# Performance work log

Hardware: AMD Instinct MI355X
Metric: run time of the kernel (lower is better)

Reference implementation:

```python
import jax, jax.numpy as jnp
import numpy as np

B, N, D, H = 4, 2048, 256, 4
NT, ET = 5, 6
HEAD = D // H


def _linear_params(k, fan_in, fan_out):
    # torch nn.Linear default init: U(-1/sqrt(fan_in), 1/sqrt(fan_in)) for W and b
    bound = 1.0 / np.sqrt(fan_in)
    kw, kb = jax.random.split(k)
    W = jax.random.uniform(kw, (fan_in, fan_out), minval=-bound, maxval=bound, dtype=jnp.float32)
    b = jax.random.uniform(kb, (fan_out,), minval=-bound, maxval=bound, dtype=jnp.float32)
    return W, b


def setup_inputs() -> dict:
    key = jax.random.key(0)
    ks = jax.random.split(key, 10)
    Wq, bq = _linear_params(ks[0], D, D)
    Wk, bk = _linear_params(ks[1], D, D)
    Wv, bv = _linear_params(ks[2], D, D)
    Wo, bo = _linear_params(ks[3], D, D)
    return {
        "nodes": jax.random.normal(ks[4], (B, N, D), dtype=jnp.float32),
        "node_types": jax.random.randint(ks[5], (B, N), 0, NT, dtype=jnp.int32),
        "edge_types": jax.random.randint(ks[6], (B, N, N), 0, ET, dtype=jnp.int32),
        "adjacency": jax.random.randint(ks[7], (B, N, N), 0, 2).astype(jnp.float32),
        "node_type_embed": jax.random.normal(ks[8], (NT, D), dtype=jnp.float32),  # nn.Embedding ~ N(0,1)
        "edge_type_embed": jax.random.normal(ks[9], (ET, H), dtype=jnp.float32),
        "Wq": Wq, "bq": bq, "Wk": Wk, "bk": bk, "Wv": Wv, "bv": bv, "Wo": Wo, "bo": bo,
        "ln_g": jnp.ones((D,), jnp.float32),
        "ln_b": jnp.zeros((D,), jnp.float32),
    }


def reference(nodes, node_types, edge_types, adjacency, node_type_embed, edge_type_embed,
              Wq, bq, Wk, bk, Wv, bv, Wo, bo, ln_g, ln_b):
    # add node-type embeddings (residual below uses the typed nodes, as in the torch code)
    x = nodes + node_type_embed[node_types]                      # [B,N,D]

    def split_heads(t):
        return t.reshape(B, N, H, HEAD).transpose(0, 2, 1, 3)    # [B,H,N,HEAD]

    Q = split_heads(x @ Wq + bq)
    K = split_heads(x @ Wk + bk)
    V = split_heads(x @ Wv + bv)

    scores = jnp.einsum('bhnd,bhmd->bhnm', Q, K) / np.sqrt(HEAD).astype(np.float32)

    # edge-type bias: [B,N,N,H] -> [B,H,N,N]
    scores = scores + jnp.transpose(edge_type_embed[edge_types], (0, 3, 1, 2))

    # type-match soft mask: match -> +0.1, mismatch -> -0.05  (== tm*0.15 - 0.05)
    tm = (node_types[:, :, None] == node_types[:, None, :]).astype(jnp.float32)
    scores = scores + (tm * 0.15 - 0.05)[:, None]

    # adjacency hard mask
    scores = scores + ((1.0 - adjacency) * -1e9)[:, None]

    attn = jax.nn.softmax(scores, axis=-1)                        # [B,H,N,N]
    ctx = jnp.einsum('bhnm,bhmd->bhnd', attn, V)
    ctx = ctx.transpose(0, 2, 1, 3).reshape(B, N, D)

    out = ctx @ Wo + bo
    y = x + out
    mu = jnp.mean(y, axis=-1, keepdims=True)
    var = jnp.var(y, axis=-1, keepdims=True)
    y = (y - mu) * jax.lax.rsqrt(var + 1e-5) * ln_g + ln_b
    return y, attn
```

## Files before the change

### kernel.cpp

```cpp
#include <hip/hip_runtime.h>

#define Bsz 4
#define Nn 2048
#define Dd 256
#define Hh 4
#define HD 64
#define NTt 5
#define ETt 6
#define LOG2E 1.4426950408889634f
#define MSUB 24.0f
#define SCLQ 0.18033688011112042f

typedef float f32x4 __attribute__((ext_vector_type(4)));
typedef __bf16 bf16x8 __attribute__((ext_vector_type(8)));
typedef unsigned int u32x4 __attribute__((ext_vector_type(4)));
typedef short s16x4 __attribute__((ext_vector_type(4)));
typedef unsigned short u16;
typedef unsigned char u8;
typedef unsigned int uint;

static __device__ __forceinline__ u16 f2bf(float f) {
  unsigned int u = __builtin_bit_cast(unsigned int, f);
  u = (u + 0x7fffu + ((u >> 16) & 1u)) >> 16;
  return (u16)u;
}

static __device__ __forceinline__ bf16x8 ld8(const u16* p) {
  return __builtin_bit_cast(bf16x8, *(const u32x4*)p);
}

static __device__ __forceinline__ void stage16(const void* g, void* l) {
  __builtin_amdgcn_global_load_lds(
      (const __attribute__((address_space(1))) uint*)g,
      (__attribute__((address_space(3))) uint*)l, 16, 0, 0);
}

#define MFMA16(a, b, c) __builtin_amdgcn_mfma_f32_16x16x32_bf16((a), (b), (c), 0, 0, 0)

#define OFF_X      0u
#define OFF_XBF    8388608u
#define OFF_WQKVT  12582912u
#define OFF_WOT    12976128u
#define OFF_BQKV   13107200u
#define OFF_Q      13110272u
#define OFF_K      17304576u
#define OFF_V      21498880u
#define OFF_VT     25693184u
#define OFF_CTX    29887488u
#define OFF_CODES  34081792u

__global__ void pack_kernel(const float* Wq, const float* Wk, const float* Wv,
                            const float* Wo, const float* bq, const float* bk,
                            const float* bv, u16* wqkvT, u16* woT, float* bqkv) {
  int tid = blockIdx.x * 256 + threadIdx.x;
  if (tid < 196608) {
    int c = tid >> 8, k = tid & 255;
    int which = c >> 8, cc = c & 255;
    const float* W = (which == 0) ? Wq : ((which == 1) ? Wk : Wv);
    wqkvT[tid] = f2bf(W[k * 256 + cc]);
  } else if (tid < 262144) {
    int t2 = tid - 196608;
    int c = t2 >> 8, k = t2 & 255;
    woT[t2] = f2bf(Wo[k * 256 + c]);
  } else if (tid < 262912) {
    int c = tid - 262144;
    int which = c >> 8, cc = c & 255;
    bqkv[c] = (which == 0) ? bq[cc] : ((which == 1) ? bk[cc] : bv[cc]);
  }
}

__global__ void embed_kernel(const float* nodes, const int* node_types,
                             const float* nte, float* xf, u16* xbf) {
  int t = blockIdx.x * 256 + threadIdx.x;
  int flat = t * 4;
  int bn = flat >> 8, d0 = flat & 255;
  int nt = node_types[bn];
  float4 nv = *(const float4*)(nodes + flat);
  float4 ev = *(const float4*)(nte + nt * 256 + d0);
  float4 x4;
  x4.x = nv.x + ev.x; x4.y = nv.y + ev.y; x4.z = nv.z + ev.z; x4.w = nv.w + ev.w;
  *(float4*)(xf + flat) = x4;
  ushort4 xb;
  xb.x = f2bf(x4.x); xb.y = f2bf(x4.y); xb.z = f2bf(x4.z); xb.w = f2bf(x4.w);
  *(ushort4*)(xbf + flat) = xb;
}

__global__ __launch_bounds__(256) void maskpack_kernel(
    const int* node_types, const int* edge_types, const float* adjacency,
    u8* codes) {
  int t = blockIdx.x * 256 + threadIdx.x;
  int lane = t & 63;
  int kt = (t >> 6) & 31;
  int qt = (t >> 11) & 127;
  int b = t >> 18;
  int l15 = lane & 15, l4 = lane >> 4;
  const int* etb = edge_types + (size_t)b * Nn * Nn;
  const float* adjb = adjacency + (size_t)b * Nn * Nn;
  const int* ntb = node_types + b * Nn;
  int qrow = qt * 16 + l15;
  int ntq = ntb[qrow];
  const int* etr = etb + (size_t)qrow * Nn;
  const float* adr = adjb + (size_t)qrow * Nn;
  unsigned int wds[4];
#pragma unroll
  for (int ks = 0; ks < 4; ++ks) {
    int k0 = kt * 64 + ks * 16 + l4 * 4;
    int4 et4 = *(const int4*)(etr + k0);
    float4 a4 = *(const float4*)(adr + k0);
    int4 nt4 = *(const int4*)(ntb + k0);
    int e[4] = {et4.x, et4.y, et4.z, et4.w};
    int n[4] = {nt4.x, nt4.y, nt4.z, nt4.w};
    float a[4] = {a4.x, a4.y, a4.z, a4.w};
    unsigned int acc = 0;
#pragma unroll
    for (int j = 0; j < 4; ++j) {
      int code = e[j] + ((ntq == n[j]) ? 6 : 0) + ((a[j] != 0.0f) ? 12 : 0);
      acc |= (unsigned int)(code * 4) << (8 * j);
    }
    wds[ks] = acc;
  }
  u32x4 out = {wds[0], wds[1], wds[2], wds[3]};
  *(u32x4*)(codes + (size_t)t * 16) = out;
}

__global__ __launch_bounds__(256) void qkv_kernel(const u16* xbf, const u16* wqkvT,
                                                  const float* bqkv,
                                                  u16* Qb, u16* Kb, u16* Vb) {
  int cb = blockIdx.x;
  int rb = blockIdx.y;
  int w = threadIdx.x >> 6, lane = threadIdx.x & 63;
  int l15 = lane & 15, l4 = lane >> 4;
  int row0 = rb * 64 + w * 16;
  int col0 = cb * 64;
  const u16* xr = xbf + (size_t)(row0 + l15) * 256;
  f32x4 acc[4];
#pragma unroll
  for (int i = 0; i < 4; ++i) acc[i] = (f32x4){0.f, 0.f, 0.f, 0.f};
#pragma unroll
  for (int kst = 0; kst < 8; ++kst) {
    int k0 = kst * 32 + l4 * 8;
    bf16x8 a = ld8(xr + k0);
#pragma unroll
    for (int cs = 0; cs < 4; ++cs) {
      int col = col0 + cs * 16 + l15;
      bf16x8 bw = ld8(wqkvT + (size_t)col * 256 + k0);
      acc[cs] = MFMA16(a, bw, acc[cs]);
    }
  }
#pragma unroll
  for (int cs = 0; cs < 4; ++cs) {
    int col = col0 + cs * 16 + l15;
    float bias = bqkv[col];
    int which = col >> 8, c = col & 255;
    int h = c >> 6, hd = c & 63;
    float scale = (which == 0) ? SCLQ : 1.0f;
    u16* dst = (which == 0) ? Qb : ((which == 1) ? Kb : Vb);
#pragma unroll
    for (int j = 0; j < 4; ++j) {
      int row = row0 + l4 * 4 + j;
      int bb = row >> 11, n = row & 2047;
      dst[(size_t)(((bb * Hh + h) * Nn + n)) * HD + hd] = f2bf((acc[cs][j] + bias) * scale);
    }
  }
}

__global__ __launch_bounds__(256) void vtrans_kernel(const u16* Vb, u16* Vtb) {
  int bh = blockIdx.y;
  int d = threadIdx.x & 63;
  int nc = threadIdx.x >> 6;
  int n0 = blockIdx.x * 64 + nc * 16;
  const u16* Vp = Vb + (size_t)bh * Nn * HD;
  union { u16 a[16]; u32x4 v[2]; } tmp;
#pragma unroll
  for (int i = 0; i < 16; ++i) tmp.a[i] = Vp[(size_t)(n0 + i) * HD + d];
  u16* dst = Vtb + ((size_t)bh * HD + d) * Nn + n0;
  *(u32x4*)dst = tmp.v[0];
  *(u32x4*)(dst + 8) = tmp.v[1];
}

__global__ __launch_bounds__(256) void attn_kernel(
    const u16* Qb, const u16* Kb, const u16* Vtb, const u8* codes,
    const float* ee_g, float* attn_out, u16* ctx_ws) {
  __shared__ __align__(16) char kls[2][8192];
  __shared__ __align__(16) char vls[2][8192];
  __shared__ __align__(16) char pls[4][2048];

  int bid0 = blockIdx.x;
  int bid = ((bid0 & 7) << 6) | (bid0 >> 3);
  int qt64 = bid & 31;
  int h = (bid >> 5) & 3;
  int b = bid >> 7;
  int w = threadIdx.x >> 6, lane = threadIdx.x & 63;
  int l15 = lane & 15, l4 = lane >> 4;
  int q0 = qt64 * 64 + w * 16;

  float lutv = 0.f;
  {
    int ln = lane;
    int et = ln - 6 * (ln / 6);
    int tm = (ln / 6) & 1;
    int adj = ln / 12;
    if (ln < 24)
      lutv = (ee_g[et * Hh + h] + (tm ? 0.10f : -0.05f)) * LOG2E +
             (adj ? 0.f : -1.442695041e9f) - MSUB;
  }
  int lut_i = __float_as_int(lutv);

  const u16* Qp = Qb + (size_t)((b * Hh + h) * Nn + q0 + l15) * HD;
  bf16x8 bq0 = ld8(Qp + l4 * 8);
  bf16x8 bq1 = ld8(Qp + 32 + l4 * 8);

  const char* Kg = (const char*)(Kb + (size_t)(b * Hh + h) * Nn * HD);
  const char* Vg = (const char*)(Vtb + (size_t)(b * Hh + h) * HD * Nn);
  const u32x4* cp = (const u32x4*)codes + ((size_t)(b * 128 + (q0 >> 4)) * 32) * 64;

  int oT0 = w * 2048 + lane * 16;
  int oT1 = oT0 + 1024;
  int ksw0 = oT0 ^ (((oT0 >> 7) & 7) << 4);
  int ksw1 = oT1 ^ (((oT1 >> 7) & 7) << 4);
  const char* VgR0 = Vg + (size_t)(oT0 >> 7) * (Nn * 2) + (ksw0 & 127);
  const char* VgR1 = Vg + (size_t)(oT1 >> 7) * (Nn * 2) + (ksw1 & 127);

  int sw = (l15 & 7) << 4;
  int ra = (l15 * 128 + l4 * 16) ^ sw;
  int qa = q0 + l15;

  stage16(Kg + ksw0, (char*)kls + w * 2048);
  stage16(Kg + ksw1, (char*)kls + w * 2048 + 1024);
  u32x4 cw = cp[lane];
  __syncthreads();

  float accl = 0.f;
#pragma unroll 1
  for (int kt = 0; kt < 32; ++kt) {
    int cb = kt & 1, nb = cb ^ 1;
    u32x4 cwn = cw;
    if (kt < 31) {
      const char* Kn = Kg + (size_t)(kt + 1) * 8192;
      stage16(Kn + ksw0, (char*)kls + nb * 8192 + w * 2048);
      stage16(Kn + ksw1, (char*)kls + nb * 8192 + w * 2048 + 1024);
      cwn = cp[(kt + 1) * 64 + lane];
    }
    __builtin_amdgcn_sched_barrier(0);
    const char* kcur = (const char*)kls + cb * 8192;
#pragma unroll
    for (int ks = 0; ks < 4; ++ks) {
      unsigned int cword = cw[ks];
      f32x4 acc;
#pragma unroll
      for (int j = 0; j < 4; ++j) {
        int c4 = (cword >> (8 * j)) & 0xFF;
        acc[j] = __int_as_float(__builtin_amdgcn_ds_bpermute(c4, lut_i));
      }
      acc = MFMA16(ld8((const u16*)(kcur + ra + ks * 2048)), bq0, acc);
      acc = MFMA16(ld8((const u16*)(kcur + (ra ^ 64) + ks * 2048)), bq1, acc);
      accl += (__builtin_amdgcn_exp2f(acc[0]) + __builtin_amdgcn_exp2f(acc[1])) +
              (__builtin_amdgcn_exp2f(acc[2]) + __builtin_amdgcn_exp2f(acc[3]));
    }
    asm volatile("s_waitcnt vmcnt(1) lgkmcnt(0)" ::: "memory");
    __builtin_amdgcn_s_barrier();
    cw = cwn;
  }
  accl += __shfl_xor(accl, 16);
  accl += __shfl_xor(accl, 32);
  bool zrow = (accl == 0.0f);
  float pscale = zrow ? 0.0f : 1.0f / accl;
  float pbias = zrow ? (1.0f / 2048.0f) : 0.0f;

  float* attb = attn_out + (size_t)(b * Hh + h) * Nn * Nn + (size_t)qa * Nn;
  char* pwave = (char*)pls + w * 2048;
  int pwbase = l15 * 128;
  f32x4 ctx[4];
#pragma unroll
  for (int i = 0; i < 4; ++i) ctx[i] = (f32x4){0.f, 0.f, 0.f, 0.f};

  stage16(Kg + ksw0, (char*)kls + w * 2048);
  stage16(Kg + ksw1, (char*)kls + w * 2048 + 1024);
  stage16(VgR0, (char*)vls + w * 2048);
  stage16(VgR1, (char*)vls + w * 2048 + 1024);
  cw = cp[lane];
  __syncthreads();

#pragma unroll 1
  for (int kt = 0; kt < 32; ++kt) {
    int cb = kt & 1, nb = cb ^ 1;
    u32x4 cwn = cw;
    if (kt < 31) {
      const char* Kn = Kg + (size_t)(kt + 1) * 8192;
      stage16(Kn + ksw0, (char*)kls + nb * 8192 + w * 2048);
      stage16(Kn + ksw1, (char*)kls + nb * 8192 + w * 2048 + 1024);
      stage16(VgR0 + (size_t)(kt + 1) * 128, (char*)vls + nb * 8192 + w * 2048);
      stage16(VgR1 + (size_t)(kt + 1) * 128, (char*)vls + nb * 8192 + w * 2048 + 1024);
      cwn = cp[(kt + 1) * 64 + lane];
    }
    __builtin_amdgcn_sched_barrier(0);
    const char* kcur = (const char*)kls + cb * 8192;
    const char* vcur = (const char*)vls + cb * 8192;
#pragma unroll
    for (int ks = 0; ks < 4; ++ks) {
      unsigned int cword = cw[ks];
      f32x4 acc;
#pragma unroll
      for (int j = 0; j < 4; ++j) {
        int c4 = (cword >> (8 * j)) & 0xFF;
        acc[j] = __int_as_float(__builtin_amdgcn_ds_bpermute(c4, lut_i));
      }
      acc = MFMA16(ld8((const u16*)(kcur + ra + ks * 2048)), bq0, acc);
      acc = MFMA16(ld8((const u16*)(kcur + (ra ^ 64) + ks * 2048)), bq1, acc);
      f32x4 p;
#pragma unroll
      for (int j = 0; j < 4; ++j)
        p[j] = __builtin_amdgcn_exp2f(acc[j]) * pscale + pbias;
      __builtin_nontemporal_store(p, (f32x4*)(attb + kt * 64 + ks * 16 + l4 * 4));
      s16x4 pb;
#pragma unroll
      for (int j = 0; j < 4; ++j)
        pb[j] = (short)__builtin_bit_cast(u16, (__bf16)p[j]);
      *(s16x4*)(pwave + pwbase + ((ks * 32 + l4 * 8) ^ sw)) = pb;
    }
    bf16x8 pa0 = ld8((const u16*)(pwave + pwbase + ((l4 * 16) ^ sw)));
    bf16x8 pa1 = ld8((const u16*)(pwave + pwbase + ((l4 * 16 + 64) ^ sw)));
#pragma unroll
    for (int ds_ = 0; ds_ < 4; ++ds_) {
      bf16x8 v0 = ld8((const u16*)(vcur + ra + ds_ * 2048));
      bf16x8 v1 = ld8((const u16*)(vcur + (ra ^ 64) + ds_ * 2048));
      ctx[ds_] = MFMA16(pa0, v0, ctx[ds_]);
      ctx[ds_] = MFMA16(pa1, v1, ctx[ds_]);
    }
    asm volatile("s_waitcnt vmcnt(5) lgkmcnt(0)" ::: "memory");
    __builtin_amdgcn_s_barrier();
    cw = cwn;
  }

#pragma unroll
  for (int ds_ = 0; ds_ < 4; ++ds_) {
    int col = h * 64 + ds_ * 16 + l15;
#pragma unroll
    for (int j = 0; j < 4; ++j) {
      int qrow = q0 + l4 * 4 + j;
      ctx_ws[(size_t)(b * Nn + qrow) * Dd + col] = f2bf(ctx[ds_][j]);
    }
  }
}

__global__ __launch_bounds__(256) void outln_kernel(const u16* ctxb, const u16* woT,
                                                    const float* bo, const float* xf,
                                                    const float* ln_g, const float* ln_b,
                                                    float* yout) {
  __shared__ float ytile[32][257];
  __shared__ float muS[32], rvS[32];
  int bm0 = blockIdx.x * 32;
  int w = threadIdx.x >> 6, lane = threadIdx.x & 63;
  int l15 = lane & 15, l4 = lane >> 4;
  f32x4 acc[2][4];
#pragma unroll
  for (int q = 0; q < 2; ++q)
#pragma unroll
    for (int i = 0; i < 4; ++i) acc[q][i] = (f32x4){0.f, 0.f, 0.f, 0.f};
#pragma unroll
  for (int kst = 0; kst < 8; ++kst) {
    int k0 = kst * 32 + l4 * 8;
    bf16x8 a0 = ld8(ctxb + (size_t)(bm0 + l15) * 256 + k0);
    bf16x8 a1 = ld8(ctxb + (size_t)(bm0 + 16 + l15) * 256 + k0);
#pragma unroll
    for (int ds_ = 0; ds_ < 4; ++ds_) {
      bf16x8 bw = ld8(woT + (size_t)(w * 64 + ds_ * 16 + l15) * 256 + k0);
      acc[0][ds_] = MFMA16(a0, bw, acc[0][ds_]);
      acc[1][ds_] = MFMA16(a1, bw, acc[1][ds_]);
    }
  }
#pragma unroll
  for (int qs = 0; qs < 2; ++qs)
#pragma unroll
    for (int ds_ = 0; ds_ < 4; ++ds_) {
      int col = w * 64 + ds_ * 16 + l15;
      float bof = bo[col];
#pragma unroll
      for (int j = 0; j < 4; ++j) {
        int row = qs * 16 + l4 * 4 + j;
        ytile[row][col] = acc[qs][ds_][j] + bof + xf[(size_t)(bm0 + row) * 256 + col];
      }
    }
  __syncthreads();
  int row = threadIdx.x >> 3, seg = threadIdx.x & 7;
  float ps = 0.f, pq = 0.f;
#pragma unroll
  for (int c = 0; c < 32; ++c) {
    float v = ytile[row][seg * 32 + c];
    ps += v; pq += v * v;
  }
  ps += __shfl_xor(ps, 1); pq += __shfl_xor(pq, 1);
  ps += __shfl_xor(ps, 2); pq += __shfl_xor(pq, 2);
  ps += __shfl_xor(ps, 4); pq += __shfl_xor(pq, 4);
  if (seg == 0) {
    float mu = ps * (1.0f / 256.0f);
    muS[row] = mu;
    rvS[row] = rsqrtf(pq * (1.0f / 256.0f) - mu * mu + 1e-5f);
  }
  __syncthreads();
  float mu = muS[row], rv = rvS[row];
  float* yr = yout + (size_t)(bm0 + row) * 256;
#pragma unroll
  for (int c0 = 0; c0 < 32; c0 += 4) {
    int c = seg * 32 + c0;
    float4 o;
    o.x = (ytile[row][c + 0] - mu) * rv * ln_g[c + 0] + ln_b[c + 0];
    o.y = (ytile[row][c + 1] - mu) * rv * ln_g[c + 1] + ln_b[c + 1];
    o.z = (ytile[row][c + 2] - mu) * rv * ln_g[c + 2] + ln_b[c + 2];
    o.w = (ytile[row][c + 3] - mu) * rv * ln_g[c + 3] + ln_b[c + 3];
    *(float4*)(yr + c) = o;
  }
}

extern "C" void kernel_launch(void* const* d_in, const int* in_sizes, int n_in,
                              void* d_out, int out_size, void* d_ws, size_t ws_size,
                              hipStream_t stream) {
  const float* nodes = (const float*)d_in[0];
  const int* node_types = (const int*)d_in[1];
  const int* edge_types = (const int*)d_in[2];
  const float* adjacency = (const float*)d_in[3];
  const float* nte = (const float*)d_in[4];
  const float* ee = (const float*)d_in[5];
  const float* Wq = (const float*)d_in[6];
  const float* bq = (const float*)d_in[7];
  const float* Wk = (const float*)d_in[8];
  const float* bk = (const float*)d_in[9];
  const float* Wv = (const float*)d_in[10];
  const float* bv = (const float*)d_in[11];
  const float* Wo = (const float*)d_in[12];
  const float* bo = (const float*)d_in[13];
  const float* ln_g = (const float*)d_in[14];
  const float* ln_b = (const float*)d_in[15];

  float* y = (float*)d_out;
  float* attn = y + (size_t)Bsz * Nn * Dd;

  char* ws = (char*)d_ws;
  float* xf = (float*)(ws + OFF_X);
  u16* xbf = (u16*)(ws + OFF_XBF);
  u16* wqkvT = (u16*)(ws + OFF_WQKVT);
  u16* woT = (u16*)(ws + OFF_WOT);
  float* bqkv = (float*)(ws + OFF_BQKV);
  u16* Qb = (u16*)(ws + OFF_Q);
  u16* Kb = (u16*)(ws + OFF_K);
  u16* Vb = (u16*)(ws + OFF_V);
  u16* Vtb = (u16*)(ws + OFF_VT);
  u16* ctxb = (u16*)(ws + OFF_CTX);
  u8* codes = (u8*)(ws + OFF_CODES);

  pack_kernel<<<1027, 256, 0, stream>>>(Wq, Wk, Wv, Wo, bq, bk, bv, wqkvT, woT, bqkv);
  embed_kernel<<<2048, 256, 0, stream>>>(nodes, node_types, nte, xf, xbf);
  maskpack_kernel<<<4096, 256, 0, stream>>>(node_types, edge_types, adjacency, codes);
  qkv_kernel<<<dim3(12, 128), 256, 0, stream>>>(xbf, wqkvT, bqkv, Qb, Kb, Vb);
  vtrans_kernel<<<dim3(32, 16), 256, 0, stream>>>(Vb, Vtb);
  attn_kernel<<<512, 256, 0, stream>>>(Qb, Kb, Vtb, codes, ee, attn, ctxb);
  outln_kernel<<<256, 256, 0, stream>>>(ctxb, woT, bo, xf, ln_g, ln_b, y);
}
```

Measured before the change: 193.2 us.

## Use single-wave attention blocks loading K/V directly from global; fuse V transpose into QKV

The attention kernel becomes one 64-thread wave per 16-query tile, loading K and V fragments straight from global memory into registers instead of double-buffering them through LDS with barriers. The V transpose kernel is removed: the QKV projection now writes V directly in transposed layout. This drops one launch and all block-level syncs and LDS staging. In exchange, K/V reuse across the four waves of a block is lost, so more global/L2 traffic is generated, and the transposed V stores are scattered.

```diff
diff --git a/kernel.cpp b/kernel.cpp
--- a/kernel.cpp
+++ b/kernel.cpp
@@ -27,12 +27,6 @@
 
 static __device__ __forceinline__ bf16x8 ld8(const u16* p) {
   return __builtin_bit_cast(bf16x8, *(const u32x4*)p);
-}
-
-static __device__ __forceinline__ void stage16(const void* g, void* l) {
-  __builtin_amdgcn_global_load_lds(
-      (const __attribute__((address_space(1))) uint*)g,
-      (__attribute__((address_space(3))) uint*)l, 16, 0, 0);
 }
 
 #define MFMA16(a, b, c) __builtin_amdgcn_mfma_f32_16x16x32_bf16((a), (b), (c), 0, 0, 0)
@@ -125,7 +119,7 @@
 
 __global__ __launch_bounds__(256) void qkv_kernel(const u16* xbf, const u16* wqkvT,
                                                   const float* bqkv,
-                                                  u16* Qb, u16* Kb, u16* Vb) {
+                                                  u16* Qb, u16* Kb, u16* Vtb) {
   int cb = blockIdx.x;
   int rb = blockIdx.y;
   int w = threadIdx.x >> 6, lane = threadIdx.x & 63;
@@ -154,45 +148,35 @@
     int which = col >> 8, c = col & 255;
     int h = c >> 6, hd = c & 63;
     float scale = (which == 0) ? SCLQ : 1.0f;
-    u16* dst = (which == 0) ? Qb : ((which == 1) ? Kb : Vb);
 #pragma unroll
     for (int j = 0; j < 4; ++j) {
       int row = row0 + l4 * 4 + j;
       int bb = row >> 11, n = row & 2047;
-      dst[(size_t)(((bb * Hh + h) * Nn + n)) * HD + hd] = f2bf((acc[cs][j] + bias) * scale);
-    }
-  }
-}
-
-__global__ __launch_bounds__(256) void vtrans_kernel(const u16* Vb, u16* Vtb) {
-  int bh = blockIdx.y;
-  int d = threadIdx.x & 63;
-  int nc = threadIdx.x >> 6;
-  int n0 = blockIdx.x * 64 + nc * 16;
-  const u16* Vp = Vb + (size_t)bh * Nn * HD;
-  union { u16 a[16]; u32x4 v[2]; } tmp;
-#pragma unroll
-  for (int i = 0; i < 16; ++i) tmp.a[i] = Vp[(size_t)(n0 + i) * HD + d];
-  u16* dst = Vtb + ((size_t)bh * HD + d) * Nn + n0;
-  *(u32x4*)dst = tmp.v[0];
-  *(u32x4*)(dst + 8) = tmp.v[1];
-}
-
-__global__ __launch_bounds__(256) void attn_kernel(
+      u16 val = f2bf((acc[cs][j] + bias) * scale);
+      if (which == 2)
+        Vtb[((size_t)((bb * Hh + h) * HD + hd)) * Nn + n] = val;
+      else if (which == 0)
+        Qb[(size_t)(((bb * Hh + h) * Nn + n)) * HD + hd] = val;
+      else
+        Kb[(size_t)(((bb * Hh + h) * Nn + n)) * HD + hd] = val;
+    }
+  }
+}
+
+__global__ __launch_bounds__(64) void attn_kernel(
     const u16* Qb, const u16* Kb, const u16* Vtb, const u8* codes,
     const float* ee_g, float* attn_out, u16* ctx_ws) {
-  __shared__ __align__(16) char kls[2][8192];
-  __shared__ __align__(16) char vls[2][8192];
-  __shared__ __align__(16) char pls[4][2048];
+  __shared__ __align__(16) char pls[2048];
 
   int bid0 = blockIdx.x;
-  int bid = ((bid0 & 7) << 6) | (bid0 >> 3);
-  int qt64 = bid & 31;
-  int h = (bid >> 5) & 3;
-  int b = bid >> 7;
-  int w = threadIdx.x >> 6, lane = threadIdx.x & 63;
+  int bid = ((bid0 & 7) << 8) | (bid0 >> 3);
+  int qt = bid & 127;
+  int h = (bid >> 7) & 3;
+  int b = bid >> 9;
+  int lane = threadIdx.x & 63;
   int l15 = lane & 15, l4 = lane >> 4;
-  int q0 = qt64 * 64 + w * 16;
+  int q0 = qt * 16;
+  int bh = b * Hh + h;
 
   float lutv = 0.f;
   {
@@ -206,59 +190,38 @@
   }
   int lut_i = __float_as_int(lutv);
 
-  const u16* Qp = Qb + (size_t)((b * Hh + h) * Nn + q0 + l15) * HD;
+  const u16* Qp = Qb + (size_t)(bh * Nn + q0 + l15) * HD;
   bf16x8 bq0 = ld8(Qp + l4 * 8);
   bf16x8 bq1 = ld8(Qp + 32 + l4 * 8);
 
-  const char* Kg = (const char*)(Kb + (size_t)(b * Hh + h) * Nn * HD);
-  const char* Vg = (const char*)(Vtb + (size_t)(b * Hh + h) * HD * Nn);
-  const u32x4* cp = (const u32x4*)codes + ((size_t)(b * 128 + (q0 >> 4)) * 32) * 64;
-
-  int oT0 = w * 2048 + lane * 16;
-  int oT1 = oT0 + 1024;
-  int ksw0 = oT0 ^ (((oT0 >> 7) & 7) << 4);
-  int ksw1 = oT1 ^ (((oT1 >> 7) & 7) << 4);
-  const char* VgR0 = Vg + (size_t)(oT0 >> 7) * (Nn * 2) + (ksw0 & 127);
-  const char* VgR1 = Vg + (size_t)(oT1 >> 7) * (Nn * 2) + (ksw1 & 127);
-
-  int sw = (l15 & 7) << 4;
-  int ra = (l15 * 128 + l4 * 16) ^ sw;
-  int qa = q0 + l15;
-
-  stage16(Kg + ksw0, (char*)kls + w * 2048);
-  stage16(Kg + ksw1, (char*)kls + w * 2048 + 1024);
-  u32x4 cw = cp[lane];
-  __syncthreads();
-
+  const u16* Kg = Kb + (size_t)bh * Nn * HD + l15 * HD + l4 * 8;
+  const u16* Vgl = Vtb + (size_t)bh * HD * Nn + (size_t)l15 * Nn + l4 * 8;
+  const u32x4* cp = (const u32x4*)codes + ((size_t)(b * 128 + qt) * 32) * 64 + lane;
+
+  u32x4 cw = cp[0];
   float accl = 0.f;
 #pragma unroll 1
   for (int kt = 0; kt < 32; ++kt) {
-    int cb = kt & 1, nb = cb ^ 1;
-    u32x4 cwn = cw;
-    if (kt < 31) {
-      const char* Kn = Kg + (size_t)(kt + 1) * 8192;
-      stage16(Kn + ksw0, (char*)kls + nb * 8192 + w * 2048);
-      stage16(Kn + ksw1, (char*)kls + nb * 8192 + w * 2048 + 1024);
-      cwn = cp[(kt + 1) * 64 + lane];
-    }
-    __builtin_amdgcn_sched_barrier(0);
-    const char* kcur = (const char*)kls + cb * 8192;
+    u32x4 cwn = cp[(size_t)(((kt + 1) & 31)) * 64];
+    const u16* kp = Kg + (size_t)kt * 4096;
+    bf16x8 kf[8];
+#pragma unroll
+    for (int i = 0; i < 8; ++i) kf[i] = ld8(kp + (i >> 1) * 1024 + (i & 1) * 32);
+    float a0 = 0.f, a1 = 0.f;
 #pragma unroll
     for (int ks = 0; ks < 4; ++ks) {
       unsigned int cword = cw[ks];
       f32x4 acc;
 #pragma unroll
-      for (int j = 0; j < 4; ++j) {
-        int c4 = (cword >> (8 * j)) & 0xFF;
-        acc[j] = __int_as_float(__builtin_amdgcn_ds_bpermute(c4, lut_i));
-      }
-      acc = MFMA16(ld8((const u16*)(kcur + ra + ks * 2048)), bq0, acc);
-      acc = MFMA16(ld8((const u16*)(kcur + (ra ^ 64) + ks * 2048)), bq1, acc);
-      accl += (__builtin_amdgcn_exp2f(acc[0]) + __builtin_amdgcn_exp2f(acc[1])) +
-              (__builtin_amdgcn_exp2f(acc[2]) + __builtin_amdgcn_exp2f(acc[3]));
-    }
-    asm volatile("s_waitcnt vmcnt(1) lgkmcnt(0)" ::: "memory");
-    __builtin_amdgcn_s_barrier();
+      for (int j = 0; j < 4; ++j)
+        acc[j] = __int_as_float(
+            __builtin_amdgcn_ds_bpermute((cword >> (8 * j)) & 0xFF, lut_i));
+      acc = MFMA16(kf[ks * 2], bq0, acc);
+      acc = MFMA16(kf[ks * 2 + 1], bq1, acc);
+      a0 += __builtin_amdgcn_exp2f(acc[0]) + __builtin_amdgcn_exp2f(acc[2]);
+      a1 += __builtin_amdgcn_exp2f(acc[1]) + __builtin_amdgcn_exp2f(acc[3]);
+    }
+    accl += a0 + a1;
     cw = cwn;
   }
   accl += __shfl_xor(accl, 16);
@@ -267,46 +230,35 @@
   float pscale = zrow ? 0.0f : 1.0f / accl;
   float pbias = zrow ? (1.0f / 2048.0f) : 0.0f;
 
-  float* attb = attn_out + (size_t)(b * Hh + h) * Nn * Nn + (size_t)qa * Nn;
-  char* pwave = (char*)pls + w * 2048;
+  float* attb = attn_out + (size_t)bh * Nn * Nn + (size_t)(q0 + l15) * Nn;
   int pwbase = l15 * 128;
+  int sw = (l15 & 7) << 4;
   f32x4 ctx[4];
 #pragma unroll
   for (int i = 0; i < 4; ++i) ctx[i] = (f32x4){0.f, 0.f, 0.f, 0.f};
 
-  stage16(Kg + ksw0, (char*)kls + w * 2048);
-  stage16(Kg + ksw1, (char*)kls + w * 2048 + 1024);
-  stage16(VgR0, (char*)vls + w * 2048);
-  stage16(VgR1, (char*)vls + w * 2048 + 1024);
-  cw = cp[lane];
-  __syncthreads();
-
+  cw = cp[0];
 #pragma unroll 1
   for (int kt = 0; kt < 32; ++kt) {
-    int cb = kt & 1, nb = cb ^ 1;
-    u32x4 cwn = cw;
-    if (kt < 31) {
-      const char* Kn = Kg + (size_t)(kt + 1) * 8192;
-      stage16(Kn + ksw0, (char*)kls + nb * 8192 + w * 2048);
-      stage16(Kn + ksw1, (char*)kls + nb * 8192 + w * 2048 + 1024);
-      stage16(VgR0 + (size_t)(kt + 1) * 128, (char*)vls + nb * 8192 + w * 2048);
-      stage16(VgR1 + (size_t)(kt + 1) * 128, (char*)vls + nb * 8192 + w * 2048 + 1024);
-      cwn = cp[(kt + 1) * 64 + lane];
-    }
-    __builtin_amdgcn_sched_barrier(0);
-    const char* kcur = (const char*)kls + cb * 8192;
-    const char* vcur = (const char*)vls + cb * 8192;
+    u32x4 cwn = cp[(size_t)(((kt + 1) & 31)) * 64];
+    const u16* kp = Kg + (size_t)kt * 4096;
+    bf16x8 kf[8];
+#pragma unroll
+    for (int i = 0; i < 8; ++i) kf[i] = ld8(kp + (i >> 1) * 1024 + (i & 1) * 32);
+    const u16* vp = Vgl + kt * 64;
+    bf16x8 vf[8];
+#pragma unroll
+    for (int i = 0; i < 8; ++i) vf[i] = ld8(vp + (size_t)(i >> 1) * 16 * Nn + (i & 1) * 32);
 #pragma unroll
     for (int ks = 0; ks < 4; ++ks) {
       unsigned int cword = cw[ks];
       f32x4 acc;
 #pragma unroll
-      for (int j = 0; j < 4; ++j) {
-        int c4 = (cword >> (8 * j)) & 0xFF;
-        acc[j] = __int_as_float(__builtin_amdgcn_ds_bpermute(c4, lut_i));
-      }
-      acc = MFMA16(ld8((const u16*)(kcur + ra + ks * 2048)), bq0, acc);
-      acc = MFMA16(ld8((const u16*)(kcur + (ra ^ 64) + ks * 2048)), bq1, acc);
+      for (int j = 0; j < 4; ++j)
+        acc[j] = __int_as_float(
+            __builtin_amdgcn_ds_bpermute((cword >> (8 * j)) & 0xFF, lut_i));
+      acc = MFMA16(kf[ks * 2], bq0, acc);
+      acc = MFMA16(kf[ks * 2 + 1], bq1, acc);
       f32x4 p;
 #pragma unroll
       for (int j = 0; j < 4; ++j)
@@ -316,19 +268,15 @@
 #pragma unroll
       for (int j = 0; j < 4; ++j)
         pb[j] = (short)__builtin_bit_cast(u16, (__bf16)p[j]);
-      *(s16x4*)(pwave + pwbase + ((ks * 32 + l4 * 8) ^ sw)) = pb;
-    }
-    bf16x8 pa0 = ld8((const u16*)(pwave + pwbase + ((l4 * 16) ^ sw)));
-    bf16x8 pa1 = ld8((const u16*)(pwave + pwbase + ((l4 * 16 + 64) ^ sw)));
+      *(s16x4*)(pls + pwbase + ((ks * 32 + l4 * 8) ^ sw)) = pb;
+    }
+    bf16x8 pa0 = ld8((const u16*)(pls + pwbase + ((l4 * 16) ^ sw)));
+    bf16x8 pa1 = ld8((const u16*)(pls + pwbase + ((l4 * 16 + 64) ^ sw)));
 #pragma unroll
     for (int ds_ = 0; ds_ < 4; ++ds_) {
-      bf16x8 v0 = ld8((const u16*)(vcur + ra + ds_ * 2048));
-      bf16x8 v1 = ld8((const u16*)(vcur + (ra ^ 64) + ds_ * 2048));
-      ctx[ds_] = MFMA16(pa0, v0, ctx[ds_]);
-      ctx[ds_] = MFMA16(pa1, v1, ctx[ds_]);
-    }
-    asm volatile("s_waitcnt vmcnt(5) lgkmcnt(0)" ::: "memory");
-    __builtin_amdgcn_s_barrier();
+      ctx[ds_] = MFMA16(pa0, vf[ds_ * 2], ctx[ds_]);
+      ctx[ds_] = MFMA16(pa1, vf[ds_ * 2 + 1], ctx[ds_]);
+    }
     cw = cwn;
   }
 
@@ -443,7 +391,6 @@
   float* bqkv = (float*)(ws + OFF_BQKV);
   u16* Qb = (u16*)(ws + OFF_Q);
   u16* Kb = (u16*)(ws + OFF_K);
-  u16* Vb = (u16*)(ws + OFF_V);
   u16* Vtb = (u16*)(ws + OFF_VT);
   u16* ctxb = (u16*)(ws + OFF_CTX);
   u8* codes = (u8*)(ws + OFF_CODES);
@@ -451,8 +398,7 @@
   pack_kernel<<<1027, 256, 0, stream>>>(Wq, Wk, Wv, Wo, bq, bk, bv, wqkvT, woT, bqkv);
   embed_kernel<<<2048, 256, 0, stream>>>(nodes, node_types, nte, xf, xbf);
   maskpack_kernel<<<4096, 256, 0, stream>>>(node_types, edge_types, adjacency, codes);
-  qkv_kernel<<<dim3(12, 128), 256, 0, stream>>>(xbf, wqkvT, bqkv, Qb, Kb, Vb);
-  vtrans_kernel<<<dim3(32, 16), 256, 0, stream>>>(Vb, Vtb);
-  attn_kernel<<<512, 256, 0, stream>>>(Qb, Kb, Vtb, codes, ee, attn, ctxb);
+  qkv_kernel<<<dim3(12, 128), 256, 0, stream>>>(xbf, wqkvT, bqkv, Qb, Kb, Vtb);
+  attn_kernel<<<2048, 64, 0, stream>>>(Qb, Kb, Vtb, codes, ee, attn, ctxb);
   outln_kernel<<<256, 256, 0, stream>>>(ctxb, woT, bo, xf, ln_g, ln_b, y);
 }
```

Result: slower. 269.6 us (+39.6%).

## Write V transposed from QKV GEMM and split attention into 32-row query blocks

Applied to the files above, without the earlier changes.

The QKV projection now writes V directly in head-dim-major layout, which removes the separate transpose kernel and its extra round trip through memory. The attention kernel now runs 1024 blocks of 128 threads (two waves, 32 query rows each) instead of 512 blocks of 256 threads, with launch bounds asking for four blocks per CU. Each wave stages a larger share of every K/V tile. The aim is better load balance and occupancy across CUs. The cost is that each K/V tile is now loaded by twice as many blocks, and the strided scalar V stores in the GEMM epilogue are poorly coalesced.

```diff
diff --git a/kernel.cpp b/kernel.cpp
--- a/kernel.cpp
+++ b/kernel.cpp
@@ -125,7 +125,7 @@
 
 __global__ __launch_bounds__(256) void qkv_kernel(const u16* xbf, const u16* wqkvT,
                                                   const float* bqkv,
-                                                  u16* Qb, u16* Kb, u16* Vb) {
+                                                  u16* Qb, u16* Kb, u16* Vtb) {
   int cb = blockIdx.x;
   int rb = blockIdx.y;
   int w = threadIdx.x >> 6, lane = threadIdx.x & 63;
@@ -154,45 +154,37 @@
     int which = col >> 8, c = col & 255;
     int h = c >> 6, hd = c & 63;
     float scale = (which == 0) ? SCLQ : 1.0f;
-    u16* dst = (which == 0) ? Qb : ((which == 1) ? Kb : Vb);
 #pragma unroll
     for (int j = 0; j < 4; ++j) {
       int row = row0 + l4 * 4 + j;
       int bb = row >> 11, n = row & 2047;
-      dst[(size_t)(((bb * Hh + h) * Nn + n)) * HD + hd] = f2bf((acc[cs][j] + bias) * scale);
-    }
-  }
-}
-
-__global__ __launch_bounds__(256) void vtrans_kernel(const u16* Vb, u16* Vtb) {
-  int bh = blockIdx.y;
-  int d = threadIdx.x & 63;
-  int nc = threadIdx.x >> 6;
-  int n0 = blockIdx.x * 64 + nc * 16;
-  const u16* Vp = Vb + (size_t)bh * Nn * HD;
-  union { u16 a[16]; u32x4 v[2]; } tmp;
-#pragma unroll
-  for (int i = 0; i < 16; ++i) tmp.a[i] = Vp[(size_t)(n0 + i) * HD + d];
-  u16* dst = Vtb + ((size_t)bh * HD + d) * Nn + n0;
-  *(u32x4*)dst = tmp.v[0];
-  *(u32x4*)(dst + 8) = tmp.v[1];
-}
-
-__global__ __launch_bounds__(256) void attn_kernel(
+      u16 val = f2bf((acc[cs][j] + bias) * scale);
+      if (which == 2)
+        Vtb[((size_t)((bb * Hh + h) * HD + hd)) * Nn + n] = val;
+      else if (which == 0)
+        Qb[(size_t)(((bb * Hh + h) * Nn + n)) * HD + hd] = val;
+      else
+        Kb[(size_t)(((bb * Hh + h) * Nn + n)) * HD + hd] = val;
+    }
+  }
+}
+
+__global__ __launch_bounds__(128, 4) void attn_kernel(
     const u16* Qb, const u16* Kb, const u16* Vtb, const u8* codes,
     const float* ee_g, float* attn_out, u16* ctx_ws) {
   __shared__ __align__(16) char kls[2][8192];
   __shared__ __align__(16) char vls[2][8192];
-  __shared__ __align__(16) char pls[4][2048];
+  __shared__ __align__(16) char pls[2][2048];
 
   int bid0 = blockIdx.x;
-  int bid = ((bid0 & 7) << 6) | (bid0 >> 3);
-  int qt64 = bid & 31;
-  int h = (bid >> 5) & 3;
-  int b = bid >> 7;
+  int bid = ((bid0 & 7) << 7) | (bid0 >> 3);
+  int qt32 = bid & 63;
+  int h = (bid >> 6) & 3;
+  int b = bid >> 8;
   int w = threadIdx.x >> 6, lane = threadIdx.x & 63;
   int l15 = lane & 15, l4 = lane >> 4;
-  int q0 = qt64 * 64 + w * 16;
+  int q0 = qt32 * 32 + w * 16;
+  int bh = b * Hh + h;
 
   float lutv = 0.f;
   {
@@ -206,27 +198,30 @@
   }
   int lut_i = __float_as_int(lutv);
 
-  const u16* Qp = Qb + (size_t)((b * Hh + h) * Nn + q0 + l15) * HD;
+  const u16* Qp = Qb + (size_t)(bh * Nn + q0 + l15) * HD;
   bf16x8 bq0 = ld8(Qp + l4 * 8);
   bf16x8 bq1 = ld8(Qp + 32 + l4 * 8);
 
-  const char* Kg = (const char*)(Kb + (size_t)(b * Hh + h) * Nn * HD);
-  const char* Vg = (const char*)(Vtb + (size_t)(b * Hh + h) * HD * Nn);
+  const char* Kg = (const char*)(Kb + (size_t)bh * Nn * HD);
+  const char* Vg = (const char*)(Vtb + (size_t)bh * HD * Nn);
   const u32x4* cp = (const u32x4*)codes + ((size_t)(b * 128 + (q0 >> 4)) * 32) * 64;
 
-  int oT0 = w * 2048 + lane * 16;
-  int oT1 = oT0 + 1024;
-  int ksw0 = oT0 ^ (((oT0 >> 7) & 7) << 4);
-  int ksw1 = oT1 ^ (((oT1 >> 7) & 7) << 4);
-  const char* VgR0 = Vg + (size_t)(oT0 >> 7) * (Nn * 2) + (ksw0 & 127);
-  const char* VgR1 = Vg + (size_t)(oT1 >> 7) * (Nn * 2) + (ksw1 & 127);
+  int oS[4], kswS[4];
+  const char* VgR[4];
+#pragma unroll
+  for (int i = 0; i < 4; ++i) {
+    int o = w * 4096 + i * 1024 + lane * 16;
+    int s = o ^ (((o >> 7) & 7) << 4);
+    oS[i] = o;
+    kswS[i] = s;
+    VgR[i] = Vg + (size_t)(o >> 7) * (Nn * 2) + (s & 127);
+  }
 
   int sw = (l15 & 7) << 4;
   int ra = (l15 * 128 + l4 * 16) ^ sw;
-  int qa = q0 + l15;
-
-  stage16(Kg + ksw0, (char*)kls + w * 2048);
-  stage16(Kg + ksw1, (char*)kls + w * 2048 + 1024);
+
+#pragma unroll
+  for (int i = 0; i < 4; ++i) stage16(Kg + kswS[i], (char*)kls + oS[i]);
   u32x4 cw = cp[lane];
   __syncthreads();
 
@@ -237,8 +232,8 @@
     u32x4 cwn = cw;
     if (kt < 31) {
       const char* Kn = Kg + (size_t)(kt + 1) * 8192;
-      stage16(Kn + ksw0, (char*)kls + nb * 8192 + w * 2048);
-      stage16(Kn + ksw1, (char*)kls + nb * 8192 + w * 2048 + 1024);
+#pragma unroll
+      for (int i = 0; i < 4; ++i) stage16(Kn + kswS[i], (char*)kls + nb * 8192 + oS[i]);
       cwn = cp[(kt + 1) * 64 + lane];
     }
     __builtin_amdgcn_sched_barrier(0);
@@ -248,10 +243,9 @@
       unsigned int cword = cw[ks];
       f32x4 acc;
 #pragma unroll
-      for (int j = 0; j < 4; ++j) {
-        int c4 = (cword >> (8 * j)) & 0xFF;
-        acc[j] = __int_as_float(__builtin_amdgcn_ds_bpermute(c4, lut_i));
-      }
+      for (int j = 0; j < 4; ++j)
+        acc[j] = __int_as_float(
+            __builtin_amdgcn_ds_bpermute((cword >> (8 * j)) & 0xFF, lut_i));
       acc = MFMA16(ld8((const u16*)(kcur + ra + ks * 2048)), bq0, acc);
       acc = MFMA16(ld8((const u16*)(kcur + (ra ^ 64) + ks * 2048)), bq1, acc);
       accl += (__builtin_amdgcn_exp2f(acc[0]) + __builtin_amdgcn_exp2f(acc[1])) +
@@ -267,17 +261,18 @@
   float pscale = zrow ? 0.0f : 1.0f / accl;
   float pbias = zrow ? (1.0f / 2048.0f) : 0.0f;
 
-  float* attb = attn_out + (size_t)(b * Hh + h) * Nn * Nn + (size_t)qa * Nn;
+  float* attb = attn_out + (size_t)bh * Nn * Nn + (size_t)(q0 + l15) * Nn;
   char* pwave = (char*)pls + w * 2048;
   int pwbase = l15 * 128;
   f32x4 ctx[4];
 #pragma unroll
   for (int i = 0; i < 4; ++i) ctx[i] = (f32x4){0.f, 0.f, 0.f, 0.f};
 
-  stage16(Kg + ksw0, (char*)kls + w * 2048);
-  stage16(Kg + ksw1, (char*)kls + w * 2048 + 1024);
-  stage16(VgR0, (char*)vls + w * 2048);
-  stage16(VgR1, (char*)vls + w * 2048 + 1024);
+#pragma unroll
+  for (int i = 0; i < 4; ++i) {
+    stage16(Kg + kswS[i], (char*)kls + oS[i]);
+    stage16(VgR[i], (char*)vls + oS[i]);
+  }
   cw = cp[lane];
   __syncthreads();
 
@@ -287,10 +282,11 @@
     u32x4 cwn = cw;
     if (kt < 31) {
       const char* Kn = Kg + (size_t)(kt + 1) * 8192;
-      stage16(Kn + ksw0, (char*)kls + nb * 8192 + w * 2048);
-      stage16(Kn + ksw1, (char*)kls + nb * 8192 + w * 2048 + 1024);
-      stage16(VgR0 + (size_t)(kt + 1) * 128, (char*)vls + nb * 8192 + w * 2048);
-      stage16(VgR1 + (size_t)(kt + 1) * 128, (char*)vls + nb * 8192 + w * 2048 + 1024);
+#pragma unroll
+      for (int i = 0; i < 4; ++i) {
+        stage16(Kn + kswS[i], (char*)kls + nb * 8192 + oS[i]);
+        stage16(VgR[i] + (size_t)(kt + 1) * 128, (char*)vls + nb * 8192 + oS[i]);
+      }
       cwn = cp[(kt + 1) * 64 + lane];
     }
     __builtin_amdgcn_sched_barrier(0);
@@ -301,10 +297,9 @@
       unsigned int cword = cw[ks];
       f32x4 acc;
 #pragma unroll
-      for (int j = 0; j < 4; ++j) {
-        int c4 = (cword >> (8 * j)) & 0xFF;
-        acc[j] = __int_as_float(__builtin_amdgcn_ds_bpermute(c4, lut_i));
-      }
+      for (int j = 0; j < 4; ++j)
+        acc[j] = __int_as_float(
+            __builtin_amdgcn_ds_bpermute((cword >> (8 * j)) & 0xFF, lut_i));
       acc = MFMA16(ld8((const u16*)(kcur + ra + ks * 2048)), bq0, acc);
       acc = MFMA16(ld8((const u16*)(kcur + (ra ^ 64) + ks * 2048)), bq1, acc);
       f32x4 p;
@@ -443,7 +438,6 @@
   float* bqkv = (float*)(ws + OFF_BQKV);
   u16* Qb = (u16*)(ws + OFF_Q);
   u16* Kb = (u16*)(ws + OFF_K);
-  u16* Vb = (u16*)(ws + OFF_V);
   u16* Vtb = (u16*)(ws + OFF_VT);
   u16* ctxb = (u16*)(ws + OFF_CTX);
   u8* codes = (u8*)(ws + OFF_CODES);
@@ -451,8 +445,7 @@
   pack_kernel<<<1027, 256, 0, stream>>>(Wq, Wk, Wv, Wo, bq, bk, bv, wqkvT, woT, bqkv);
   embed_kernel<<<2048, 256, 0, stream>>>(nodes, node_types, nte, xf, xbf);
   maskpack_kernel<<<4096, 256, 0, stream>>>(node_types, edge_types, adjacency, codes);
-  qkv_kernel<<<dim3(12, 128), 256, 0, stream>>>(xbf, wqkvT, bqkv, Qb, Kb, Vb);
-  vtrans_kernel<<<dim3(32, 16), 256, 0, stream>>>(Vb, Vtb);
-  attn_kernel<<<512, 256, 0, stream>>>(Qb, Kb, Vtb, codes, ee, attn, ctxb);
+  qkv_kernel<<<dim3(12, 128), 256, 0, stream>>>(xbf, wqkvT, bqkv, Qb, Kb, Vtb);
+  attn_kernel<<<1024, 128, 0, stream>>>(Qb, Kb, Vtb, codes, ee, attn, ctxb);
   outln_kernel<<<256, 256, 0, stream>>>(ctxb, woT, bo, xf, ln_g, ln_b, y);
 }
```

Measured after the change: 203.7 us. 5.5% more time.

## Triple-buffer K/V LDS staging with prefetch distance two in attention passes

Applied to the files above, without the earlier changes.

Grows the K and V shared-memory staging buffers from two to three slots and prefetches the tile two iterations ahead in both the row-sum pass and the probability/context pass. The vmcnt wait counts are adjusted so outstanding global loads can span an extra iteration, hiding more memory latency. In exchange, LDS use per block rises, which may lower occupancy, and the hand-tuned waitcnt values are fragile.

```diff
diff --git a/kernel.cpp b/kernel.cpp
--- a/kernel.cpp
+++ b/kernel.cpp
@@ -181,8 +181,8 @@
 __global__ __launch_bounds__(256) void attn_kernel(
     const u16* Qb, const u16* Kb, const u16* Vtb, const u8* codes,
     const float* ee_g, float* attn_out, u16* ctx_ws) {
-  __shared__ __align__(16) char kls[2][8192];
-  __shared__ __align__(16) char vls[2][8192];
+  __shared__ __align__(16) char kls[3][8192];
+  __shared__ __align__(16) char vls[3][8192];
   __shared__ __align__(16) char pls[4][2048];
 
   int bid0 = blockIdx.x;
@@ -193,6 +193,7 @@
   int w = threadIdx.x >> 6, lane = threadIdx.x & 63;
   int l15 = lane & 15, l4 = lane >> 4;
   int q0 = qt64 * 64 + w * 16;
+  int bh = b * Hh + h;
 
   float lutv = 0.f;
   {
@@ -206,12 +207,12 @@
   }
   int lut_i = __float_as_int(lutv);
 
-  const u16* Qp = Qb + (size_t)((b * Hh + h) * Nn + q0 + l15) * HD;
+  const u16* Qp = Qb + (size_t)(bh * Nn + q0 + l15) * HD;
   bf16x8 bq0 = ld8(Qp + l4 * 8);
   bf16x8 bq1 = ld8(Qp + 32 + l4 * 8);
 
-  const char* Kg = (const char*)(Kb + (size_t)(b * Hh + h) * Nn * HD);
-  const char* Vg = (const char*)(Vtb + (size_t)(b * Hh + h) * HD * Nn);
+  const char* Kg = (const char*)(Kb + (size_t)bh * Nn * HD);
+  const char* Vg = (const char*)(Vtb + (size_t)bh * HD * Nn);
   const u32x4* cp = (const u32x4*)codes + ((size_t)(b * 128 + (q0 >> 4)) * 32) * 64;
 
   int oT0 = w * 2048 + lane * 16;
@@ -223,23 +224,32 @@
 
   int sw = (l15 & 7) << 4;
   int ra = (l15 * 128 + l4 * 16) ^ sw;
-  int qa = q0 + l15;
-
-  stage16(Kg + ksw0, (char*)kls + w * 2048);
-  stage16(Kg + ksw1, (char*)kls + w * 2048 + 1024);
+
   u32x4 cw = cp[lane];
-  __syncthreads();
+  __builtin_amdgcn_sched_barrier(0);
+  {
+    char* kd = (char*)kls + w * 2048;
+    stage16(Kg + ksw0, kd);
+    stage16(Kg + ksw1, kd + 1024);
+    stage16(Kg + 8192 + ksw0, kd + 8192);
+    stage16(Kg + 8192 + ksw1, kd + 8192 + 1024);
+  }
+  asm volatile("s_waitcnt vmcnt(2) lgkmcnt(0)" ::: "memory");
+  __builtin_amdgcn_s_barrier();
 
   float accl = 0.f;
+  int cb = 0;
 #pragma unroll 1
   for (int kt = 0; kt < 32; ++kt) {
-    int cb = kt & 1, nb = cb ^ 1;
     u32x4 cwn = cw;
-    if (kt < 31) {
-      const char* Kn = Kg + (size_t)(kt + 1) * 8192;
-      stage16(Kn + ksw0, (char*)kls + nb * 8192 + w * 2048);
-      stage16(Kn + ksw1, (char*)kls + nb * 8192 + w * 2048 + 1024);
-      cwn = cp[(kt + 1) * 64 + lane];
+    if (kt < 31) cwn = cp[(kt + 1) * 64 + lane];
+    __builtin_amdgcn_sched_barrier(0);
+    if (kt < 30) {
+      int nb = cb ? cb - 1 : 2;
+      const char* Kn = Kg + (size_t)(kt + 2) * 8192;
+      char* kd = (char*)kls + nb * 8192 + w * 2048;
+      stage16(Kn + ksw0, kd);
+      stage16(Kn + ksw1, kd + 1024);
     }
     __builtin_amdgcn_sched_barrier(0);
     const char* kcur = (const char*)kls + cb * 8192;
@@ -248,18 +258,21 @@
       unsigned int cword = cw[ks];
       f32x4 acc;
 #pragma unroll
-      for (int j = 0; j < 4; ++j) {
-        int c4 = (cword >> (8 * j)) & 0xFF;
-        acc[j] = __int_as_float(__builtin_amdgcn_ds_bpermute(c4, lut_i));
-      }
+      for (int j = 0; j < 4; ++j)
+        acc[j] = __int_as_float(
+            __builtin_amdgcn_ds_bpermute((cword >> (8 * j)) & 0xFF, lut_i));
       acc = MFMA16(ld8((const u16*)(kcur + ra + ks * 2048)), bq0, acc);
       acc = MFMA16(ld8((const u16*)(kcur + (ra ^ 64) + ks * 2048)), bq1, acc);
       accl += (__builtin_amdgcn_exp2f(acc[0]) + __builtin_amdgcn_exp2f(acc[1])) +
               (__builtin_amdgcn_exp2f(acc[2]) + __builtin_amdgcn_exp2f(acc[3]));
     }
-    asm volatile("s_waitcnt vmcnt(1) lgkmcnt(0)" ::: "memory");
-    __builtin_amdgcn_s_barrier();
+    if (kt < 30)
+      asm volatile("s_waitcnt vmcnt(2) lgkmcnt(0)" ::: "memory");
+    else if (kt == 30)
+      asm volatile("s_waitcnt vmcnt(0) lgkmcnt(0)" ::: "memory");
+    if (kt < 31) __builtin_amdgcn_s_barrier();
     cw = cwn;
+    cb = (cb == 2) ? 0 : cb + 1;
   }
   accl += __shfl_xor(accl, 16);
   accl += __shfl_xor(accl, 32);
@@ -267,31 +280,47 @@
   float pscale = zrow ? 0.0f : 1.0f / accl;
   float pbias = zrow ? (1.0f / 2048.0f) : 0.0f;
 
-  float* attb = attn_out + (size_t)(b * Hh + h) * Nn * Nn + (size_t)qa * Nn;
+  __syncthreads();
+
+  float* attb = attn_out + (size_t)bh * Nn * Nn + (size_t)(q0 + l15) * Nn;
   char* pwave = (char*)pls + w * 2048;
   int pwbase = l15 * 128;
   f32x4 ctx[4];
 #pragma unroll
   for (int i = 0; i < 4; ++i) ctx[i] = (f32x4){0.f, 0.f, 0.f, 0.f};
 
-  stage16(Kg + ksw0, (char*)kls + w * 2048);
-  stage16(Kg + ksw1, (char*)kls + w * 2048 + 1024);
-  stage16(VgR0, (char*)vls + w * 2048);
-  stage16(VgR1, (char*)vls + w * 2048 + 1024);
   cw = cp[lane];
-  __syncthreads();
-
+  __builtin_amdgcn_sched_barrier(0);
+  {
+    char* kd = (char*)kls + w * 2048;
+    char* vd = (char*)vls + w * 2048;
+    stage16(Kg + ksw0, kd);
+    stage16(Kg + ksw1, kd + 1024);
+    stage16(VgR0, vd);
+    stage16(VgR1, vd + 1024);
+    stage16(Kg + 8192 + ksw0, kd + 8192);
+    stage16(Kg + 8192 + ksw1, kd + 8192 + 1024);
+    stage16(VgR0 + 128, vd + 8192);
+    stage16(VgR1 + 128, vd + 8192 + 1024);
+  }
+  asm volatile("s_waitcnt vmcnt(4) lgkmcnt(0)" ::: "memory");
+  __builtin_amdgcn_s_barrier();
+
+  cb = 0;
 #pragma unroll 1
   for (int kt = 0; kt < 32; ++kt) {
-    int cb = kt & 1, nb = cb ^ 1;
     u32x4 cwn = cw;
-    if (kt < 31) {
-      const char* Kn = Kg + (size_t)(kt + 1) * 8192;
-      stage16(Kn + ksw0, (char*)kls + nb * 8192 + w * 2048);
-      stage16(Kn + ksw1, (char*)kls + nb * 8192 + w * 2048 + 1024);
-      stage16(VgR0 + (size_t)(kt + 1) * 128, (char*)vls + nb * 8192 + w * 2048);
-      stage16(VgR1 + (size_t)(kt + 1) * 128, (char*)vls + nb * 8192 + w * 2048 + 1024);
-      cwn = cp[(kt + 1) * 64 + lane];
+    if (kt < 31) cwn = cp[(kt + 1) * 64 + lane];
+    __builtin_amdgcn_sched_barrier(0);
+    if (kt < 30) {
+      int nb = cb ? cb - 1 : 2;
+      const char* Kn = Kg + (size_t)(kt + 2) * 8192;
+      char* kd = (char*)kls + nb * 8192 + w * 2048;
+      char* vd = (char*)vls + nb * 8192 + w * 2048;
+      stage16(Kn + ksw0, kd);
+      stage16(Kn + ksw1, kd + 1024);
+      stage16(VgR0 + (size_t)(kt + 2) * 128, vd);
+      stage16(VgR1 + (size_t)(kt + 2) * 128, vd + 1024);
     }
     __builtin_amdgcn_sched_barrier(0);
     const char* kcur = (const char*)kls + cb * 8192;
@@ -301,10 +330,9 @@
       unsigned int cword = cw[ks];
       f32x4 acc;
 #pragma unroll
-      for (int j = 0; j < 4; ++j) {
-        int c4 = (cword >> (8 * j)) & 0xFF;
-        acc[j] = __int_as_float(__builtin_amdgcn_ds_bpermute(c4, lut_i));
-      }
+      for (int j = 0; j < 4; ++j)
+        acc[j] = __int_as_float(
+            __builtin_amdgcn_ds_bpermute((cword >> (8 * j)) & 0xFF, lut_i));
       acc = MFMA16(ld8((const u16*)(kcur + ra + ks * 2048)), bq0, acc);
       acc = MFMA16(ld8((const u16*)(kcur + (ra ^ 64) + ks * 2048)), bq1, acc);
       f32x4 p;
@@ -327,9 +355,13 @@
       ctx[ds_] = MFMA16(pa0, v0, ctx[ds_]);
       ctx[ds_] = MFMA16(pa1, v1, ctx[ds_]);
     }
-    asm volatile("s_waitcnt vmcnt(5) lgkmcnt(0)" ::: "memory");
-    __builtin_amdgcn_s_barrier();
+    if (kt < 30)
+      asm volatile("s_waitcnt vmcnt(8) lgkmcnt(0)" ::: "memory");
+    else if (kt == 30)
+      asm volatile("s_waitcnt vmcnt(4) lgkmcnt(0)" ::: "memory");
+    if (kt < 31) __builtin_amdgcn_s_barrier();
     cw = cwn;
+    cb = (cb == 2) ? 0 : cb + 1;
   }
 
 #pragma unroll
```

Measured after the change: 192.3 us. No clear change (-0.5%).
